# Kernel tuning notes

Measured on AMD Instinct MI355X. Metric: run time of the kernel, lower is better.

## Reference

```python
import jax, jax.numpy as jnp
import numpy as np

ALPHA = 2.0  # init alpha
B, N, E = 8, 100000, 3200000


def setup_inputs() -> dict:
    key = jax.random.key(0)
    k1, k2, k3, k4 = jax.random.split(key, 4)
    y = jax.random.normal(k1, (B, N), dtype=jnp.float32)
    t = jnp.zeros((1,), dtype=jnp.float32)  # unused by the math, kept for signature fidelity
    graph_edge_attr = jax.random.uniform(k2, (E,), dtype=jnp.float32)
    dist_w = jax.random.normal(k3, (E,), dtype=jnp.float32)  # distances.weight ([E,1] flattened)
    edge_index = jax.random.randint(k4, (2, E), 0, N, dtype=jnp.int64)
    return {"y": y, "t": t, "graph_edge_attr": graph_edge_attr, "dist_w": dist_w, "edge_index": edge_index}


def reference(y, t, graph_edge_attr, dist_w, edge_index):
    ei0 = edge_index[0]  # source node per edge [E]
    ei1 = edge_index[1]  # target node per edge [E]
    n = y.shape[1]
    # edge_attr = sigmoid(distances.weight) -> [E]
    edge_attr = jax.nn.sigmoid(dist_w)
    # deg = scatter_add(graph.edge_attr, edge_index[0], dim_size=N) -> [N]
    deg = jax.ops.segment_sum(graph_edge_attr, ei0, num_segments=n)
    deg_a = jnp.power(deg[ei0], ALPHA)  # [E], gathered per edge at source node
    # grad_m = sqrt(edge_attr) * -1 * min(y[:,ei1]/deg^a - y[:,ei0]/deg^a, 0) -> [B,E]
    diff = y[:, ei1] / deg_a - y[:, ei0] / deg_a
    grad_m = jnp.sqrt(edge_attr) * (-1.0) * jnp.minimum(diff, 0.0)
    # grad_norm = scatter_add(|grad_m|, ei0, dim=1, dim_size=N) -> [B,N]
    grad_norm = jnp.zeros_like(y).at[:, ei0].add(jnp.abs(grad_m))
    # run_pde is None -> return f (mask branch not taken)
    return 1.0 - grad_norm
```

## Files before the change

### kernel.cpp

```cpp
#include <hip/hip_runtime.h>
#include <hip/hip_fp16.h>

#define BATCH 8
#define S_LOG 9
#define SBUCKET 512
#define KC 256
#define CB 1024
#define TTILE 2048
#define EPT (TTILE / 256)
#define MA 8

static inline size_t alignup(size_t x) { return (x + 255) & ~(size_t)255; }

__device__ __forceinline__ unsigned bf16hi(unsigned u) {
    return (u + 0x7FFFu + ((u >> 16) & 1u)) >> 16;
}


__global__ __launch_bounds__(256)
void count_transpose_kernel(const int* __restrict__ ei0, unsigned* __restrict__ counts,
                            const float* __restrict__ y, uint4* __restrict__ yT,
                            int E, int N, int Npad) {
    __shared__ unsigned cnt[KC];
    int tid = threadIdx.x;
    if (blockIdx.x >= CB) {
        int n = (blockIdx.x - CB) * 256 + tid;
        if (n < Npad) {
            uint4 o = make_uint4(0u, 0u, 0u, 0u);
            if (n < N) {
                unsigned p[8];
#pragma unroll
                for (int b = 0; b < BATCH; ++b)
                    p[b] = bf16hi(__float_as_uint(y[(size_t)b * N + n]));
                o = make_uint4(p[0] | (p[1] << 16), p[2] | (p[3] << 16),
                               p[4] | (p[5] << 16), p[6] | (p[7] << 16));
            }
            yT[n] = o;
        }
        return;
    }
    cnt[tid] = 0;
    __syncthreads();
    int chunk = (E + CB - 1) / CB;
    int lo = blockIdx.x * chunk;
    int hi = min(lo + chunk, E);
    for (int i = lo + tid; i < hi; i += 256)
        atomicAdd(&cnt[ei0[i] >> S_LOG], 1u);
    __syncthreads();
    counts[(size_t)tid * CB + blockIdx.x] = cnt[tid];
}

__global__ __launch_bounds__(256)
void scanB1_kernel(const unsigned* __restrict__ counts, unsigned* __restrict__ base,
                   unsigned* __restrict__ tot) {
    __shared__ unsigned ssum[256];
    int k = blockIdx.x, tid = threadIdx.x;
    const uint4* row4 = (const uint4*)(counts + (size_t)k * CB);
    uint4 v = row4[tid];
    unsigned lsum = v.x + v.y + v.z + v.w;
    ssum[tid] = lsum;
    __syncthreads();
    for (int off = 1; off < 256; off <<= 1) {
        unsigned u = ssum[tid];
        unsigned a = (tid >= off) ? ssum[tid - off] : 0u;
        __syncthreads();
        ssum[tid] = u + a;
        __syncthreads();
    }
    unsigned ex = ssum[tid] - lsum;
    if (tid == 255) tot[k] = ssum[255];
    uint4 o;
    o.x = ex;
    o.y = ex + v.x;
    o.z = o.y + v.y;
    o.w = o.z + v.z;
    ((uint4*)(base + (size_t)k * CB))[tid] = o;
}

__global__ void scanC_kernel(const unsigned* __restrict__ tot,
                             unsigned* __restrict__ bb, int E, int K) {
    __shared__ unsigned sb[KC];
    int t = threadIdx.x;
    unsigned v = (t < K) ? tot[t] : 0u;
    sb[t] = v;
    __syncthreads();
    for (int off = 1; off < KC; off <<= 1) {
        unsigned u = sb[t];
        unsigned a = (t >= off) ? sb[t - off] : 0u;
        __syncthreads();
        sb[t] = u + a;
        __syncthreads();
    }
    bb[t] = sb[t] - v;
    if (t == KC - 1) bb[KC] = (unsigned)E;
}

__global__ __launch_bounds__(256)
void scatter_kernel(const int* __restrict__ ei0, const int* __restrict__ ei1,
                    const float* __restrict__ dw, const float* __restrict__ gea,
                    const unsigned* __restrict__ base, const unsigned* __restrict__ bb,
                    uint2* __restrict__ w0coef, int E) {
    __shared__ unsigned cursor[KC];
    __shared__ unsigned h[KC];
    __shared__ unsigned tstart[KC];
    __shared__ unsigned wsum[4];
    __shared__ uint2 srec[TTILE];
    __shared__ unsigned char skey[TTILE];
    int tid = threadIdx.x;
    cursor[tid] = base[(size_t)tid * CB + blockIdx.x] + bb[tid];
    int chunk = (E + CB - 1) / CB;
    int lo = blockIdx.x * chunk;
    int hi = min(lo + chunk, E);
    __syncthreads();

    for (int tileLo = lo; tileLo < hi; tileLo += TTILE) {
        int tn = min(TTILE, hi - tileLo);
        h[tid] = 0;
        __syncthreads();

        unsigned k_r[EPT], w0_r[EPT], pk_r[EPT], rk_r[EPT];
#pragma unroll
        for (int j = 0; j < EPT; ++j) {
            int off = j * 256 + tid;
            k_r[j] = 0xFFFFFFFFu;
            if (off < tn) {
                int i = tileLo + off;
                int s0v = ei0[i];
                int s1v = ei1[i];
                unsigned k = (unsigned)s0v >> S_LOG;
                unsigned s0l = (unsigned)(s0v & (SBUCKET - 1));
                k_r[j] = k;
                w0_r[j] = (unsigned)s1v | (s0l << 17);
                float sig = 1.0f / (1.0f + __expf(-dw[i]));
                unsigned cf = __float_as_uint(sqrtf(sig));
                unsigned gu = __float_as_uint(gea[i]);
                pk_r[j] = (bf16hi(cf) << 16) | bf16hi(gu);
            }
        }
#pragma unroll
        for (int j = 0; j < EPT; ++j)
            if (k_r[j] != 0xFFFFFFFFu) rk_r[j] = atomicAdd(&h[k_r[j]], 1u);
        __syncthreads();

        unsigned hv = h[tid];
        unsigned v = hv;
        unsigned lane = tid & 63;
        unsigned wv = tid >> 6;
#pragma unroll
        for (int off = 1; off < 64; off <<= 1) {
            unsigned t = __shfl_up(v, off, 64);
            if (lane >= off) v += t;
        }
        if (lane == 63) wsum[wv] = v;
        __syncthreads();
        unsigned addv = 0;
#pragma unroll
        for (unsigned w = 0; w < 4; ++w)
            if (w < wv) addv += wsum[w];
        tstart[tid] = v + addv - hv;
        __syncthreads();

#pragma unroll
        for (int j = 0; j < EPT; ++j)
            if (k_r[j] != 0xFFFFFFFFu) {
                unsigned slot = tstart[k_r[j]] + rk_r[j];
                srec[slot] = make_uint2(w0_r[j], pk_r[j]);
                skey[slot] = (unsigned char)k_r[j];
            }
        __syncthreads();

        for (int i = tid; i < tn; i += 256) {
            uint2 u = srec[i];
            unsigned k = skey[i];
            unsigned pos = cursor[k] + ((unsigned)i - tstart[k]);
            w0coef[pos] = u;
        }
        __syncthreads();
        cursor[tid] += h[tid];
        __syncthreads();
    }
}

__global__ __launch_bounds__(256)
void accum_kernel(const uint2* __restrict__ w0coef, const unsigned* __restrict__ bb,
                  const uint4* __restrict__ yT,
                  float* __restrict__ pdegp, float* __restrict__ pout,
                  int N, int Npad) {
    __shared__ uint4  y0l[SBUCKET];
    __shared__ __half2 outw[4][4][SBUCKET];
    __shared__ float  degw[4][SBUCKET];
    int k = blockIdx.x, m = blockIdx.y, tid = threadIdx.x;
    int n0 = k << S_LOG;
    unsigned lane = tid & 63;
    unsigned wv = tid >> 6;

    for (int i = tid; i < 4 * 4 * SBUCKET; i += 256)
        ((unsigned*)outw)[i] = 0u;
    for (int i = tid; i < 4 * SBUCKET; i += 256)
        ((float*)degw)[i] = 0.0f;
    for (int j = tid; j < SBUCKET; j += 256) y0l[j] = yT[n0 + j];
    unsigned lo = bb[k], hi = bb[k + 1];
    unsigned cnt = hi - lo;
    unsigned slice = (cnt + MA - 1) / MA;
    unsigned slo = lo + m * slice;
    unsigned shi = min(slo + slice, hi);
    __syncthreads();

    __half2 (*myout)[SBUCKET] = outw[wv];
    float* mydeg = degw[wv];

    unsigned i0 = slo + tid;
    uint2 z2 = make_uint2(0u, 0u);
    uint2 c0 = z2, c1 = z2, d0 = z2, d1 = z2;
    uint4 zg = make_uint4(0u, 0u, 0u, 0u);
    uint4 g0 = zg, g1 = zg;
    bool vc0 = i0 < shi,       vc1 = i0 + 256 < shi;
    bool vd0 = i0 + 512 < shi, vd1 = i0 + 768 < shi;
    if (vc0) c0 = w0coef[i0];
    if (vc1) c1 = w0coef[i0 + 256];
    if (vd0) d0 = w0coef[i0 + 512];
    if (vd1) d1 = w0coef[i0 + 768];
    if (vc0) g0 = yT[c0.x & 0x1FFFFu];
    if (vc1) g1 = yT[c1.x & 0x1FFFFu];

    while (__any(vc0)) {
        uint4 h0 = zg, h1 = zg;
        if (vd0) h0 = yT[d0.x & 0x1FFFFu];
        if (vd1) h1 = yT[d1.x & 0x1FFFFu];
        uint2 e0 = z2, e1 = z2;
        bool ve0 = i0 + 1024 < shi, ve1 = i0 + 1280 < shi;
        if (ve0) e0 = w0coef[i0 + 1024];
        if (ve1) e1 = w0coef[i0 + 1280];

#pragma unroll
        for (int half = 0; half < 2; ++half) {
            bool val = half ? vc1 : vc0;
            uint2 cc = half ? c1 : c0;
            uint4 gg = half ? g1 : g0;
            unsigned s0l = cc.x >> 17;
            unsigned long long mm = ~0ull;
#pragma unroll
            for (int b = 0; b < 9; ++b) {
                unsigned long long vb = __ballot((s0l >> b) & 1u);
                mm &= ((s0l >> b) & 1u) ? vb : ~vb;
            }
            unsigned rank = __popcll(mm & ((1ull << lane) - 1ull));
            float cf = __uint_as_float(cc.y & 0xFFFF0000u);
            float ge = __uint_as_float(cc.y << 16);
            uint4 y0r = y0l[s0l];
            float q[8];
            {
                const unsigned yw[4] = {y0r.x, y0r.y, y0r.z, y0r.w};
                const unsigned gw[4] = {gg.x, gg.y, gg.z, gg.w};
#pragma unroll
                for (int p = 0; p < 4; ++p) {
                    float ya = __uint_as_float(yw[p] << 16);
                    float yb = __uint_as_float(yw[p] & 0xFFFF0000u);
                    float ga = __uint_as_float(gw[p] << 16);
                    float gb = __uint_as_float(gw[p] & 0xFFFF0000u);
                    q[2 * p]     = cf * fmaxf(ya - ga, 0.0f);
                    q[2 * p + 1] = cf * fmaxf(yb - gb, 0.0f);
                }
            }
            unsigned r = 0;
            bool pending = val;
            while (__any(pending && rank >= r ? 1 : 0)) {
                if (pending && rank == r) {
#pragma unroll
                    for (int p = 0; p < 4; ++p) {
                        float2 f = __half22float2(myout[p][s0l]);
                        f.x += q[2 * p];
                        f.y += q[2 * p + 1];
                        myout[p][s0l] = __floats2half2_rn(f.x, f.y);
                    }
                    mydeg[s0l] += ge;
                    pending = false;
                }
                ++r;
            }
        }

        c0 = d0; c1 = d1; d0 = e0; d1 = e1;
        g0 = h0; g1 = h1;
        vc0 = vd0; vc1 = vd1; vd0 = ve0; vd1 = ve1;
        i0 += 512;
    }
    __syncthreads();

    for (int i = tid; i < SBUCKET; i += 256) {
        float d = degw[0][i] + degw[1][i] + degw[2][i] + degw[3][i];
        pdegp[(size_t)m * Npad + n0 + i] = d;
    }
    for (int i = tid; i < BATCH * SBUCKET; i += 256) {
        int b = i >> S_LOG;
        int j = i & (SBUCKET - 1);
        int p = b >> 1;
        float s = 0.0f;
#pragma unroll
        for (int w = 0; w < 4; ++w) {
            float2 f = __half22float2(outw[w][p][j]);
            s += (b & 1) ? f.y : f.x;
        }
        pout[((size_t)m * BATCH + b) * Npad + n0 + j] = s;
    }
}

__global__ __launch_bounds__(256)
void finalize_kernel(const float* __restrict__ pdegp, const float* __restrict__ pout,
                     float* __restrict__ out, int N, int Npad) {
    int n = blockIdx.x * blockDim.x + threadIdx.x;
    if (n >= N) return;
    float d = 0.0f;
#pragma unroll
    for (int m = 0; m < MA; ++m) d += pdegp[(size_t)m * Npad + n];
    float inv = 1.0f / (d * d);
#pragma unroll
    for (int b = 0; b < BATCH; ++b) {
        float s = 0.0f;
#pragma unroll
        for (int m = 0; m < MA; ++m)
            s += pout[((size_t)m * BATCH + b) * Npad + n];
        out[(size_t)b * N + n] = 1.0f - s * inv;
    }
}


__global__ void fill_one_kernel(float* __restrict__ out, int n) {
    int i = blockIdx.x * blockDim.x + threadIdx.x;
    if (i < n) out[i] = 1.0f;
}

__global__ void deg_kernel(const float* __restrict__ gea,
                           const int* __restrict__ ei0,
                           float* __restrict__ deg, int E) {
    int e = blockIdx.x * blockDim.x + threadIdx.x;
    if (e < E) atomicAdd(&deg[ei0[e]], gea[e]);
}

__global__ void edge_kernel(const float* __restrict__ y,
                            const float* __restrict__ dw,
                            const int* __restrict__ ei0,
                            const int* __restrict__ ei1,
                            const float* __restrict__ deg,
                            float* __restrict__ out,
                            int E, int N) {
    int e = blockIdx.x * blockDim.x + threadIdx.x;
    if (e >= E) return;
    int s0 = ei0[e];
    int s1 = ei1[e];
    float d = deg[s0];
    float inv = 1.0f / (d * d);
    float sig = 1.0f / (1.0f + __expf(-dw[e]));
    float coef = sqrtf(sig) * inv;
#pragma unroll
    for (int b = 0; b < BATCH; ++b) {
        float y0 = y[(size_t)b * N + s0];
        float y1 = y[(size_t)b * N + s1];
        float gm = coef * fmaxf(y0 - y1, 0.0f);
        if (gm != 0.0f) atomicAdd(&out[(size_t)b * N + s0], -gm);
    }
}


extern "C" void kernel_launch(void* const* d_in, const int* in_sizes, int n_in,
                              void* d_out, int out_size, void* d_ws, size_t ws_size,
                              hipStream_t stream) {
    const float* y   = (const float*)d_in[0];
    const float* gea = (const float*)d_in[2];
    const float* dw  = (const float*)d_in[3];
    const int*   ei  = (const int*)d_in[4];

    const int E = in_sizes[2];
    const int N = in_sizes[0] / BATCH;
    const int* ei0 = ei;
    const int* ei1 = ei + E;

    const int K = (N + SBUCKET - 1) >> S_LOG;
    const int Npad = K << S_LOG;

    size_t o_yT     = 0;
    size_t o_rcf    = o_yT     + alignup((size_t)Npad * 16);
    size_t o_counts = o_rcf    + alignup((size_t)E * 8);
    size_t o_base   = o_counts + alignup((size_t)KC * CB * 4);
    size_t o_tot    = o_base   + alignup((size_t)KC * CB * 4);
    size_t o_bb     = o_tot    + alignup((size_t)KC * 4);
    size_t o_pdegp  = o_bb     + alignup((size_t)(KC + 1) * 4);
    size_t o_pout   = o_pdegp  + alignup((size_t)MA * Npad * 4);
    size_t need     = o_pout   + alignup((size_t)MA * BATCH * Npad * 4);

    if (K <= KC && N <= 131071 && ws_size >= need) {
        char* w = (char*)d_ws;
        uint4*    yT     = (uint4*)(w + o_yT);
        uint2*    w0coef = (uint2*)(w + o_rcf);
        unsigned* counts = (unsigned*)(w + o_counts);
        unsigned* base   = (unsigned*)(w + o_base);
        unsigned* tot    = (unsigned*)(w + o_tot);
        unsigned* bb     = (unsigned*)(w + o_bb);
        float*    pdegp  = (float*)(w + o_pdegp);
        float*    pout   = (float*)(w + o_pout);

        int tb = (Npad + 255) / 256;
        count_transpose_kernel<<<CB + tb, 256, 0, stream>>>(ei0, counts, y, yT,
                                                            E, N, Npad);
        scanB1_kernel<<<K, 256, 0, stream>>>(counts, base, tot);
        scanC_kernel<<<1, KC, 0, stream>>>(tot, bb, E, K);
        scatter_kernel<<<CB, 256, 0, stream>>>(ei0, ei1, dw, gea, base, bb,
                                               w0coef, E);
        accum_kernel<<<dim3(K, MA), 256, 0, stream>>>(w0coef, bb, yT,
                                                      pdegp, pout, N, Npad);
        finalize_kernel<<<(N + 255) / 256, 256, 0, stream>>>(
            pdegp, pout, (float*)d_out, N, Npad);
    } else {
        float* deg = (float*)d_ws;
        (void)hipMemsetAsync(deg, 0, (size_t)N * sizeof(float), stream);
        fill_one_kernel<<<(out_size + 255) / 256, 256, 0, stream>>>((float*)d_out, out_size);
        deg_kernel<<<(E + 255) / 256, 256, 0, stream>>>(gea, ei0, deg, E);
        edge_kernel<<<(E + 255) / 256, 256, 0, stream>>>(y, dw, ei0, ei1, deg,
                                                         (float*)d_out, E, N);
    }
}
```

Measured before the change: 177.3 us.

## Replace LDS atomics with ballot-based warp aggregation and drop accum LDS y-cache

The count and scatter kernels now group lanes with equal bucket keys using ballot bit-matching and keep per-wavefront histograms, so each distinct bucket gets one LDS update per wavefront instead of contended per-element atomics. The scatter kernel derives per-wavefront start offsets from a combined prefix scan. In the accum kernel, the per-bucket LDS cache of source-node y values is removed and those values are instead gathered from global memory alongside the target gather. This trades LDS atomic contention and an LDS preload for extra ballot instructions and doubled global gathers, which mostly hit cache since source nodes lie in one 512-node bucket.

Result: slower. 184.0 us (+3.8%).

```diff
diff --git a/kernel.cpp b/kernel.cpp
--- a/kernel.cpp
+++ b/kernel.cpp
@@ -21,7 +21,7 @@
 void count_transpose_kernel(const int* __restrict__ ei0, unsigned* __restrict__ counts,
                             const float* __restrict__ y, uint4* __restrict__ yT,
                             int E, int N, int Npad) {
-    __shared__ unsigned cnt[KC];
+    __shared__ unsigned hw[4][KC];
     int tid = threadIdx.x;
     if (blockIdx.x >= CB) {
         int n = (blockIdx.x - CB) * 256 + tid;
@@ -39,15 +39,29 @@
         }
         return;
     }
-    cnt[tid] = 0;
+    unsigned lane = tid & 63, wv = tid >> 6;
+    for (int i = tid; i < 4 * KC; i += 256) ((unsigned*)hw)[i] = 0u;
     __syncthreads();
     int chunk = (E + CB - 1) / CB;
     int lo = blockIdx.x * chunk;
     int hi = min(lo + chunk, E);
-    for (int i = lo + tid; i < hi; i += 256)
-        atomicAdd(&cnt[ei0[i] >> S_LOG], 1u);
-    __syncthreads();
-    counts[(size_t)tid * CB + blockIdx.x] = cnt[tid];
+    for (int base_i = lo; base_i < hi; base_i += 256) {
+        int i = base_i + tid;
+        bool valid = i < hi;
+        unsigned k = valid ? ((unsigned)ei0[i] >> S_LOG) : 0u;
+        unsigned long long mm = __ballot(valid ? 1 : 0);
+#pragma unroll
+        for (int b = 0; b < 8; ++b) {
+            unsigned long long vb = __ballot((k >> b) & 1u);
+            mm &= ((k >> b) & 1u) ? vb : ~vb;
+        }
+        unsigned rank = __popcll(mm & ((1ull << lane) - 1ull));
+        unsigned gsz = __popcll(mm);
+        if (valid && rank == 0) hw[wv][k] += gsz;
+    }
+    __syncthreads();
+    counts[(size_t)tid * CB + blockIdx.x] =
+        hw[0][tid] + hw[1][tid] + hw[2][tid] + hw[3][tid];
 }
 
 __global__ __launch_bounds__(256)
@@ -101,12 +115,12 @@
                     const unsigned* __restrict__ base, const unsigned* __restrict__ bb,
                     uint2* __restrict__ w0coef, int E) {
     __shared__ unsigned cursor[KC];
-    __shared__ unsigned h[KC];
-    __shared__ unsigned tstart[KC];
+    __shared__ unsigned hw[4][KC];
     __shared__ unsigned wsum[4];
     __shared__ uint2 srec[TTILE];
     __shared__ unsigned char skey[TTILE];
     int tid = threadIdx.x;
+    unsigned lane = tid & 63, wv = tid >> 6;
     cursor[tid] = base[(size_t)tid * CB + blockIdx.x] + bb[tid];
     int chunk = (E + CB - 1) / CB;
     int lo = blockIdx.x * chunk;
@@ -115,19 +129,21 @@
 
     for (int tileLo = lo; tileLo < hi; tileLo += TTILE) {
         int tn = min(TTILE, hi - tileLo);
-        h[tid] = 0;
+        for (int i = tid; i < 4 * KC; i += 256) ((unsigned*)hw)[i] = 0u;
         __syncthreads();
 
         unsigned k_r[EPT], w0_r[EPT], pk_r[EPT], rk_r[EPT];
 #pragma unroll
         for (int j = 0; j < EPT; ++j) {
             int off = j * 256 + tid;
+            bool valid = off < tn;
             k_r[j] = 0xFFFFFFFFu;
-            if (off < tn) {
+            unsigned k = 0u;
+            if (valid) {
                 int i = tileLo + off;
                 int s0v = ei0[i];
                 int s1v = ei1[i];
-                unsigned k = (unsigned)s0v >> S_LOG;
+                k = (unsigned)s0v >> S_LOG;
                 unsigned s0l = (unsigned)(s0v & (SBUCKET - 1));
                 k_r[j] = k;
                 w0_r[j] = (unsigned)s1v | (s0l << 17);
@@ -136,34 +152,48 @@
                 unsigned gu = __float_as_uint(gea[i]);
                 pk_r[j] = (bf16hi(cf) << 16) | bf16hi(gu);
             }
-        }
-#pragma unroll
-        for (int j = 0; j < EPT; ++j)
-            if (k_r[j] != 0xFFFFFFFFu) rk_r[j] = atomicAdd(&h[k_r[j]], 1u);
-        __syncthreads();
-
-        unsigned hv = h[tid];
-        unsigned v = hv;
-        unsigned lane = tid & 63;
-        unsigned wv = tid >> 6;
-#pragma unroll
-        for (int off = 1; off < 64; off <<= 1) {
-            unsigned t = __shfl_up(v, off, 64);
-            if (lane >= off) v += t;
-        }
-        if (lane == 63) wsum[wv] = v;
-        __syncthreads();
-        unsigned addv = 0;
-#pragma unroll
-        for (unsigned w = 0; w < 4; ++w)
-            if (w < wv) addv += wsum[w];
-        tstart[tid] = v + addv - hv;
+            unsigned long long mm = __ballot(valid ? 1 : 0);
+#pragma unroll
+            for (int b = 0; b < 8; ++b) {
+                unsigned long long vb = __ballot((k >> b) & 1u);
+                mm &= ((k >> b) & 1u) ? vb : ~vb;
+            }
+            unsigned rank = __popcll(mm & ((1ull << lane) - 1ull));
+            unsigned gsz = __popcll(mm);
+            unsigned cur = 0;
+            if (valid) cur = hw[wv][k];
+            if (valid && rank == 0) hw[wv][k] = cur + gsz;
+            rk_r[j] = cur + rank;
+        }
+        __syncthreads();
+
+        unsigned h0 = hw[0][tid], h1 = hw[1][tid], h2 = hw[2][tid], h3 = hw[3][tid];
+        unsigned tot_t = h0 + h1 + h2 + h3;
+        {
+            unsigned v = tot_t;
+#pragma unroll
+            for (int off = 1; off < 64; off <<= 1) {
+                unsigned t2 = __shfl_up(v, off, 64);
+                if (lane >= off) v += t2;
+            }
+            if (lane == 63) wsum[wv] = v;
+            __syncthreads();
+            unsigned addv = 0;
+#pragma unroll
+            for (unsigned w = 0; w < 4; ++w)
+                if (w < wv) addv += wsum[w];
+            unsigned tstart = v + addv - tot_t;
+            hw[0][tid] = tstart;
+            hw[1][tid] = tstart + h0;
+            hw[2][tid] = tstart + h0 + h1;
+            hw[3][tid] = tstart + h0 + h1 + h2;
+        }
         __syncthreads();
 
 #pragma unroll
         for (int j = 0; j < EPT; ++j)
             if (k_r[j] != 0xFFFFFFFFu) {
-                unsigned slot = tstart[k_r[j]] + rk_r[j];
+                unsigned slot = hw[wv][k_r[j]] + rk_r[j];
                 srec[slot] = make_uint2(w0_r[j], pk_r[j]);
                 skey[slot] = (unsigned char)k_r[j];
             }
@@ -172,11 +202,11 @@
         for (int i = tid; i < tn; i += 256) {
             uint2 u = srec[i];
             unsigned k = skey[i];
-            unsigned pos = cursor[k] + ((unsigned)i - tstart[k]);
+            unsigned pos = cursor[k] + ((unsigned)i - hw[0][k]);
             w0coef[pos] = u;
         }
         __syncthreads();
-        cursor[tid] += h[tid];
+        cursor[tid] += tot_t;
         __syncthreads();
     }
 }
@@ -186,7 +216,6 @@
                   const uint4* __restrict__ yT,
                   float* __restrict__ pdegp, float* __restrict__ pout,
                   int N, int Npad) {
-    __shared__ uint4  y0l[SBUCKET];
     __shared__ __half2 outw[4][4][SBUCKET];
     __shared__ float  degw[4][SBUCKET];
     int k = blockIdx.x, m = blockIdx.y, tid = threadIdx.x;
@@ -198,7 +227,6 @@
         ((unsigned*)outw)[i] = 0u;
     for (int i = tid; i < 4 * SBUCKET; i += 256)
         ((float*)degw)[i] = 0.0f;
-    for (int j = tid; j < SBUCKET; j += 256) y0l[j] = yT[n0 + j];
     unsigned lo = bb[k], hi = bb[k + 1];
     unsigned cnt = hi - lo;
     unsigned slice = (cnt + MA - 1) / MA;
@@ -213,20 +241,20 @@
     uint2 z2 = make_uint2(0u, 0u);
     uint2 c0 = z2, c1 = z2, d0 = z2, d1 = z2;
     uint4 zg = make_uint4(0u, 0u, 0u, 0u);
-    uint4 g0 = zg, g1 = zg;
+    uint4 g0 = zg, g1 = zg, yg0 = zg, yg1 = zg;
     bool vc0 = i0 < shi,       vc1 = i0 + 256 < shi;
     bool vd0 = i0 + 512 < shi, vd1 = i0 + 768 < shi;
     if (vc0) c0 = w0coef[i0];
     if (vc1) c1 = w0coef[i0 + 256];
     if (vd0) d0 = w0coef[i0 + 512];
     if (vd1) d1 = w0coef[i0 + 768];
-    if (vc0) g0 = yT[c0.x & 0x1FFFFu];
-    if (vc1) g1 = yT[c1.x & 0x1FFFFu];
+    if (vc0) { g0 = yT[c0.x & 0x1FFFFu]; yg0 = yT[n0 + (c0.x >> 17)]; }
+    if (vc1) { g1 = yT[c1.x & 0x1FFFFu]; yg1 = yT[n0 + (c1.x >> 17)]; }
 
     while (__any(vc0)) {
-        uint4 h0 = zg, h1 = zg;
-        if (vd0) h0 = yT[d0.x & 0x1FFFFu];
-        if (vd1) h1 = yT[d1.x & 0x1FFFFu];
+        uint4 h0 = zg, h1 = zg, yh0 = zg, yh1 = zg;
+        if (vd0) { h0 = yT[d0.x & 0x1FFFFu]; yh0 = yT[n0 + (d0.x >> 17)]; }
+        if (vd1) { h1 = yT[d1.x & 0x1FFFFu]; yh1 = yT[n0 + (d1.x >> 17)]; }
         uint2 e0 = z2, e1 = z2;
         bool ve0 = i0 + 1024 < shi, ve1 = i0 + 1280 < shi;
         if (ve0) e0 = w0coef[i0 + 1024];
@@ -237,6 +265,7 @@
             bool val = half ? vc1 : vc0;
             uint2 cc = half ? c1 : c0;
             uint4 gg = half ? g1 : g0;
+            uint4 y0r = half ? yg1 : yg0;
             unsigned s0l = cc.x >> 17;
             unsigned long long mm = ~0ull;
 #pragma unroll
@@ -247,7 +276,6 @@
             unsigned rank = __popcll(mm & ((1ull << lane) - 1ull));
             float cf = __uint_as_float(cc.y & 0xFFFF0000u);
             float ge = __uint_as_float(cc.y << 16);
-            uint4 y0r = y0l[s0l];
             float q[8];
             {
                 const unsigned yw[4] = {y0r.x, y0r.y, y0r.z, y0r.w};
@@ -281,7 +309,7 @@
         }
 
         c0 = d0; c1 = d1; d0 = e0; d1 = e1;
-        g0 = h0; g1 = h1;
+        g0 = h0; g1 = h1; yg0 = yh0; yg1 = yh1;
         vc0 = vd0; vc1 = vd1; vd0 = ve0; vd1 = ve1;
         i0 += 512;
     }
```
